# Performance work log

Hardware: AMD Instinct MI355X
Metric: run time of the kernel (lower is better)

## Reference

```python
import jax, jax.numpy as jnp
import numpy as np

N, D, E, L = 50000, 128, 800000, 3
BN_EPS = 1e-5


def _bn(h, mean, var, gamma, beta):
    # eval-mode BatchNorm1d with running statistics
    return (h - mean) * jax.lax.rsqrt(var + BN_EPS) * gamma + beta


def setup_inputs() -> dict:
    key = jax.random.key(0)
    ks = jax.random.split(key, 16)
    x = jax.random.normal(ks[0], (N, D), dtype=jnp.float32)
    edge_index = jax.random.randint(ks[1], (2, E), 0, N, dtype=jnp.int32)
    s = 1.0 / np.sqrt(D)
    W1 = jax.random.uniform(ks[2], (L, D, 2 * D), jnp.float32, -s, s)
    b1 = jax.random.uniform(ks[3], (L, 2 * D), jnp.float32, -s, s)
    g1 = jnp.ones((L, 2 * D), jnp.float32)
    be1 = jnp.zeros((L, 2 * D), jnp.float32)
    m1 = jax.random.normal(ks[4], (L, 2 * D), jnp.float32) * 0.1
    v1 = jax.random.uniform(ks[5], (L, 2 * D), jnp.float32, 0.5, 1.5)
    s2 = 1.0 / np.sqrt(2 * D)
    W2 = jax.random.uniform(ks[6], (L, 2 * D, D), jnp.float32, -s2, s2)
    b2 = jax.random.uniform(ks[7], (L, D), jnp.float32, -s2, s2)
    eps = jnp.zeros((L,), jnp.float32)  # train_eps=True, init 0
    go = jnp.ones((L - 1, D), jnp.float32)
    bo = jnp.zeros((L - 1, D), jnp.float32)
    mo = jax.random.normal(ks[8], (L - 1, D), jnp.float32) * 0.1
    vo = jax.random.uniform(ks[9], (L - 1, D), jnp.float32, 0.5, 1.5)
    return {"x": x, "edge_index": edge_index, "W1": W1, "b1": b1, "g1": g1,
            "be1": be1, "m1": m1, "v1": v1, "W2": W2, "b2": b2, "eps": eps,
            "go": go, "bo": bo, "mo": mo, "vo": vo}


def reference(x, edge_index, W1, b1, g1, be1, m1, v1, W2, b2, eps, go, bo, mo, vo):
    src, dst = edge_index[0], edge_index[1]
    n = x.shape[0]
    h = x
    for i in range(L):
        # GINConv: (1+eps)*x_i + sum_{j in N(i)} x_j, then MLP
        agg = jax.ops.segment_sum(h[src], dst, num_segments=n)  # [N, D]
        z = (1.0 + eps[i]) * h + agg
        z = jax.nn.relu(_bn(z @ W1[i] + b1[i], m1[i], v1[i], g1[i], be1[i]))
        z = z @ W2[i] + b2[i]
        if i < L - 1:
            z = jax.nn.relu(_bn(z, mo[i], vo[i], go[i], bo[i]))
            # dropout: identity in eval mode
        h = z
    return jax.nn.log_softmax(h, axis=-1)
```

## Files before the change

### kernel.cpp

```cpp
#include <hip/hip_runtime.h>

#define N_NODES 50000
#define DIM 128
#define E_EDGES 800000
#define L_LAYERS 3
#define MTPAD 3128
#define NBUCK 98
#define BCAP 9216
#define BSHIFT 9

#define CVT_BLOCKS 6250
#define TRANS_BLOCKS 768
#define PREP_BLOCKS 5

typedef __attribute__((ext_vector_type(4))) float f32x4;
typedef __attribute__((ext_vector_type(2))) _Float16 f16x2;
typedef __attribute__((ext_vector_type(4))) _Float16 f16x4;
typedef __attribute__((ext_vector_type(8))) _Float16 f16x8;

__device__ inline unsigned int pack4_fp8(float a, float b, float c, float d) {
    int pk = __builtin_amdgcn_cvt_pk_fp8_f32(a, b, 0, false);
    pk = __builtin_amdgcn_cvt_pk_fp8_f32(c, d, pk, true);
    return (unsigned int)pk;
}

__global__ __launch_bounds__(256) void setup_kernel(
        const float4* __restrict__ x4, f16x4* __restrict__ h16o,
        unsigned int* __restrict__ h8o,
        const float* __restrict__ w1, const float* __restrict__ w2,
        _Float16* __restrict__ f1, _Float16* __restrict__ f2,
        const float* __restrict__ b1, const float* __restrict__ g1,
        const float* __restrict__ be1, const float* __restrict__ m1,
        const float* __restrict__ v1, const float* __restrict__ b2,
        const float* __restrict__ go, const float* __restrict__ bo,
        const float* __restrict__ mo, const float* __restrict__ vo,
        float* __restrict__ scale1, float* __restrict__ shift1,
        float* __restrict__ scale2, float* __restrict__ shift2,
        int* __restrict__ gcur) {
    const int b = blockIdx.x;
    const int t = threadIdx.x;
    if (b < CVT_BLOCKS) {
        int i = b * 256 + t;
        float4 v = x4[i];
        f16x4 o;
        o[0] = (_Float16)v.x; o[1] = (_Float16)v.y;
        o[2] = (_Float16)v.z; o[3] = (_Float16)v.w;
        h16o[i] = o;
        h8o[i] = pack4_fp8(v.x, v.y, v.z, v.w);
    } else if (b < CVT_BLOCKS + TRANS_BLOCKS) {
        int idx = (b - CVT_BLOCKS) * 256 + t;
        const int per = DIM * 2 * DIM;
        const int tot = L_LAYERS * per;
        const float* w;
        _Float16* f;
        int K, Nn, id;
        if (idx < tot) { w = w1; f = f1; K = DIM; Nn = 2 * DIM; id = idx; }
        else           { w = w2; f = f2; K = 2 * DIM; Nn = DIM; id = idx - tot; }
        int l = id / per;
        int r = id - l * per;
        int k = r / Nn;
        int n = r - k * Nn;
        int KS = K >> 5;
        int off = ((((n >> 4) * KS + (k >> 5)) * 4 + ((k >> 3) & 3)) * 16 + (n & 15)) * 8 + (k & 7);
        f[(size_t)l * per + off] = (_Float16)w[id];
    } else if (b < CVT_BLOCKS + TRANS_BLOCKS + PREP_BLOCKS) {
        int idx = (b - (CVT_BLOCKS + TRANS_BLOCKS)) * 256 + t;
        if (idx < L_LAYERS * 256) {
            float sv = g1[idx] * rsqrtf(v1[idx] + 1e-5f);
            scale1[idx] = sv;
            shift1[idx] = (b1[idx] - m1[idx]) * sv + be1[idx];
        }
        int idx2 = idx - L_LAYERS * 256;
        if (idx2 >= 0 && idx2 < L_LAYERS * 128) {
            int l = idx2 >> 7;
            if (l < L_LAYERS - 1) {
                float sv = go[idx2] * rsqrtf(vo[idx2] + 1e-5f);
                scale2[idx2] = sv;
                shift2[idx2] = (b2[idx2] - mo[idx2]) * sv + bo[idx2];
            } else {
                scale2[idx2] = 1.0f;
                shift2[idx2] = b2[idx2];
            }
        }
    } else {
        if (t < NBUCK) gcur[t] = t * BCAP;
    }
}


__global__ __launch_bounds__(256) void bin_kernel(const int* __restrict__ ei,
                                                  int* __restrict__ gcur,
                                                  unsigned int* __restrict__ brec) {
    __shared__ int cnt[NBUCK];
    __shared__ int off[NBUCK];
    __shared__ int gbase[NBUCK];
    __shared__ unsigned int rec[4096];
    const int t = threadIdx.x;
    const int start = blockIdx.x * 4096;
    for (int i = t; i < NBUCK; i += 256) cnt[i] = 0;
    __syncthreads();
    unsigned int myrec[16];
    unsigned int mypos[16];
    int nmine = 0;
    #pragma unroll
    for (int i = 0; i < 16; ++i) {
        int e = start + i * 256 + t;
        if (e < E_EDGES) {
            int src = ei[e];
            int dst = ei[E_EDGES + e];
            int b = dst >> BSHIFT;
            int idx = atomicAdd(&cnt[b], 1);
            myrec[i] = ((unsigned int)(dst & 511) << 16) | (unsigned int)src;
            mypos[i] = ((unsigned int)b << 16) | (unsigned int)idx;
            nmine = i + 1;
        }
    }
    __syncthreads();
    if (t == 0) {
        int s = 0;
        for (int b = 0; b < NBUCK; ++b) { off[b] = s; s += cnt[b]; }
    }
    __syncthreads();
    #pragma unroll
    for (int i = 0; i < 16; ++i) {
        if (i < nmine) {
            int b = mypos[i] >> 16;
            int idx = mypos[i] & 0xFFFF;
            rec[off[b] + idx] = myrec[i];
        }
    }
    __syncthreads();
    if (t < NBUCK && cnt[t] > 0) gbase[t] = atomicAdd(&gcur[t], cnt[t]);
    __syncthreads();
    const int wv = t >> 6, lane = t & 63;
    for (int b = wv; b < NBUCK; b += 4) {
        int c = cnt[b], o = off[b], g = gbase[b];
        for (int j = lane; j < c; j += 64)
            brec[g + j] = rec[o + j];
    }
}

__global__ __launch_bounds__(256) void bsort_kernel(const unsigned int* __restrict__ brec,
                                                    const int* __restrict__ gcur,
                                                    int* __restrict__ rowp,
                                                    unsigned short* __restrict__ col) {
    __shared__ int ncnt[512];
    __shared__ int noff[512];
    __shared__ int wsum[4];
    __shared__ unsigned short srcbuf[BCAP];
    const int b = blockIdx.x;
    const int t = threadIdx.x;
    const int lane = t & 63;
    const int wv = t >> 6;
    int pv = (t < b) ? (gcur[t] - t * BCAP) : 0;
    #pragma unroll
    for (int d = 1; d < 64; d <<= 1) pv += __shfl_xor(pv, d, 64);
    if (lane == 0) wsum[wv] = pv;
    if (b == 0 && t == 0) rowp[N_NODES] = E_EDGES;
    const int cnt = gcur[b] - b * BCAP;
    const unsigned int* r = brec + (size_t)b * BCAP;
    for (int i = t; i < 512; i += 256) ncnt[i] = 0;
    __syncthreads();
    const int cb = wsum[0] + wsum[1] + wsum[2] + wsum[3];
    for (int j = t; j < cnt; j += 256)
        atomicAdd(&ncnt[r[j] >> 16], 1);
    __syncthreads();
    int a0 = ncnt[2 * t], a1 = ncnt[2 * t + 1];
    int pair = a0 + a1;
    int inc = pair;
    #pragma unroll
    for (int d = 1; d < 64; d <<= 1) {
        int u = __shfl_up(inc, d, 64);
        if (lane >= d) inc += u;
    }
    if (lane == 63) wsum[wv] = inc;
    __syncthreads();
    int wo = 0;
    if (wv > 0) wo = wsum[0];
    if (wv > 1) wo += wsum[1];
    if (wv > 2) wo += wsum[2];
    int excl = wo + inc - pair;
    noff[2 * t] = excl;
    noff[2 * t + 1] = excl + a0;
    __syncthreads();
    const int n0 = b << BSHIFT;
    for (int i = t; i < 512; i += 256) {
        int node = n0 + i;
        if (node < N_NODES) rowp[node] = cb + noff[i];
    }
    for (int i = t; i < 512; i += 256) ncnt[i] = noff[i];
    __syncthreads();
    for (int j = t; j < cnt; j += 256) {
        unsigned int v = r[j];
        int pos = atomicAdd(&ncnt[v >> 16], 1);
        srcbuf[pos] = (unsigned short)(v & 0xFFFFu);
    }
    __syncthreads();
    unsigned short* cp = col + cb;
    for (int j = t; j < cnt; j += 256) cp[j] = srcbuf[j];
}

__global__ __launch_bounds__(256) void aggregate_kernel(
        const unsigned int* __restrict__ h16,
        const unsigned int* __restrict__ h8,
        const int* __restrict__ row, const unsigned short* __restrict__ col,
        const float* __restrict__ epsp,
        unsigned short* __restrict__ zf) {
    const int wv = threadIdx.x >> 6;
    const int lane = threadIdx.x & 63;
    const int half = lane >> 5;
    const int m = lane & 31;
    const int node = blockIdx.x * 4 + wv;
    const f16x4* __restrict__ h4 = (const f16x4*)h16;
    const float s = 1.0f + epsp[0];
    f16x4 hv = h4[(size_t)node * 32 + m];
    float h0 = (float)hv[0], h1 = (float)hv[1], h2 = (float)hv[2], h3 = (float)hv[3];
    const int self8 = (int)h8[(size_t)node * 32 + m];
    float n0 = __builtin_amdgcn_cvt_f32_fp8(self8, 0);
    float n1 = __builtin_amdgcn_cvt_f32_fp8(self8, 1);
    float n2 = __builtin_amdgcn_cvt_f32_fp8(self8, 2);
    float n3 = __builtin_amdgcn_cvt_f32_fp8(self8, 3);
    float a0 = 0.f, a1 = 0.f, a2 = 0.f, a3 = 0.f;
    const int e0 = row[node], e1 = row[node + 1];
    int pad = 0;
    for (int e = e0; e < e1; e += 16) {
        int idx[8];
        #pragma unroll
        for (int p = 0; p < 8; ++p) {
            int ee = e + 2 * p + half;
            int cl = ee < E_EDGES - 1 ? ee : E_EDGES - 1;
            int cc = col[cl];
            idx[p] = (ee < e1) ? cc : node;
        }
        pad += (e + 16 > e1) ? (e + 16 - e1) : 0;
        int w0 = (int)h8[(size_t)idx[0] * 32 + m];
        int w1 = (int)h8[(size_t)idx[1] * 32 + m];
        int w2 = (int)h8[(size_t)idx[2] * 32 + m];
        int w3 = (int)h8[(size_t)idx[3] * 32 + m];
        int w4 = (int)h8[(size_t)idx[4] * 32 + m];
        int w5 = (int)h8[(size_t)idx[5] * 32 + m];
        int w6 = (int)h8[(size_t)idx[6] * 32 + m];
        int w7 = (int)h8[(size_t)idx[7] * 32 + m];
        a0 += ((__builtin_amdgcn_cvt_f32_fp8(w0, 0) + __builtin_amdgcn_cvt_f32_fp8(w1, 0))
             + (__builtin_amdgcn_cvt_f32_fp8(w2, 0) + __builtin_amdgcn_cvt_f32_fp8(w3, 0)))
            + ((__builtin_amdgcn_cvt_f32_fp8(w4, 0) + __builtin_amdgcn_cvt_f32_fp8(w5, 0))
             + (__builtin_amdgcn_cvt_f32_fp8(w6, 0) + __builtin_amdgcn_cvt_f32_fp8(w7, 0)));
        a1 += ((__builtin_amdgcn_cvt_f32_fp8(w0, 1) + __builtin_amdgcn_cvt_f32_fp8(w1, 1))
             + (__builtin_amdgcn_cvt_f32_fp8(w2, 1) + __builtin_amdgcn_cvt_f32_fp8(w3, 1)))
            + ((__builtin_amdgcn_cvt_f32_fp8(w4, 1) + __builtin_amdgcn_cvt_f32_fp8(w5, 1))
             + (__builtin_amdgcn_cvt_f32_fp8(w6, 1) + __builtin_amdgcn_cvt_f32_fp8(w7, 1)));
        a2 += ((__builtin_amdgcn_cvt_f32_fp8(w0, 2) + __builtin_amdgcn_cvt_f32_fp8(w1, 2))
             + (__builtin_amdgcn_cvt_f32_fp8(w2, 2) + __builtin_amdgcn_cvt_f32_fp8(w3, 2)))
            + ((__builtin_amdgcn_cvt_f32_fp8(w4, 2) + __builtin_amdgcn_cvt_f32_fp8(w5, 2))
             + (__builtin_amdgcn_cvt_f32_fp8(w6, 2) + __builtin_amdgcn_cvt_f32_fp8(w7, 2)));
        a3 += ((__builtin_amdgcn_cvt_f32_fp8(w0, 3) + __builtin_amdgcn_cvt_f32_fp8(w1, 3))
             + (__builtin_amdgcn_cvt_f32_fp8(w2, 3) + __builtin_amdgcn_cvt_f32_fp8(w3, 3)))
            + ((__builtin_amdgcn_cvt_f32_fp8(w4, 3) + __builtin_amdgcn_cvt_f32_fp8(w5, 3))
             + (__builtin_amdgcn_cvt_f32_fp8(w6, 3) + __builtin_amdgcn_cvt_f32_fp8(w7, 3)));
    }
    a0 += __shfl_xor(a0, 32, 64);
    a1 += __shfl_xor(a1, 32, 64);
    a2 += __shfl_xor(a2, 32, 64);
    a3 += __shfl_xor(a3, 32, 64);
    const float fpad = (float)pad;
    float t0 = s * h0 + a0 - fpad * n0;
    float t1 = s * h1 + a1 - fpad * n1;
    float t2 = s * h2 + a2 - fpad * n2;
    float t3 = s * h3 + a3 - fpad * n3;
    if (half == 0) {
        unsigned int lo = (unsigned int)__builtin_bit_cast(unsigned short, (_Float16)t0)
                        | ((unsigned int)__builtin_bit_cast(unsigned short, (_Float16)t1) << 16);
        unsigned int hi = (unsigned int)__builtin_bit_cast(unsigned short, (_Float16)t2)
                        | ((unsigned int)__builtin_bit_cast(unsigned short, (_Float16)t3) << 16);
        int mt = node >> 4, r16 = node & 15;
        int ks = m >> 3, quad = (m >> 1) & 3, j0 = (m & 1) * 4;
        size_t zo = (((size_t)(mt * 4 + ks)) * 4 + quad) * 128 + r16 * 8 + j0;
        uint2 pk; pk.x = lo; pk.y = hi;
        *(uint2*)(zf + zo) = pk;
    }
}

__global__ __launch_bounds__(256) void mlp_kernel(
        const _Float16* __restrict__ zf,
        const _Float16* __restrict__ w1f, const _Float16* __restrict__ w2f,
        const float* __restrict__ scale1, const float* __restrict__ shift1,
        const float* __restrict__ scale2, const float* __restrict__ shift2,
        int last,
        unsigned short* __restrict__ h16out, unsigned char* __restrict__ h8out,
        float* __restrict__ lsout) {
    __shared__ _Float16 wbuf[16384];
    __shared__ _Float16 tbuf[4][2][2048];
    const int tid = threadIdx.x;
    const int wave = tid >> 6;
    const int lane = tid & 63;
    const int quad = lane >> 4;
    const int l16 = lane & 15;
    const int mt0 = blockIdx.x * 8 + wave * 2;

    f16x8 ah[2][4];
    #pragma unroll
    for (int tt = 0; tt < 2; ++tt)
        #pragma unroll
        for (int ks = 0; ks < 4; ++ks)
            ah[tt][ks] = *(const f16x8*)(zf + (((size_t)((mt0 + tt) * 4 + ks)) << 9) + lane * 8);

    f32x4 acc2[2][8] = {};
    #pragma unroll
    for (int c = 0; c < 2; ++c) {
        {
            const _Float16* g = w1f + c * 16384 + tid * 8;
            _Float16* l = wbuf + tid * 8;
            #pragma unroll
            for (int j = 0; j < 8; ++j)
                *(f16x8*)(l + j * 2048) = *(const f16x8*)(g + j * 2048);
        }
        __syncthreads();
        #pragma unroll
        for (int ntl = 0; ntl < 8; ++ntl) {
            f32x4 acc[2] = {};
            #pragma unroll
            for (int ks = 0; ks < 4; ++ks) {
                f16x8 bfr = *(const f16x8*)&wbuf[(ntl * 4 + ks) * 512 + lane * 8];
                acc[0] = __builtin_amdgcn_mfma_f32_16x16x32_f16(ah[0][ks], bfr, acc[0], 0, 0, 0);
                acc[1] = __builtin_amdgcn_mfma_f32_16x16x32_f16(ah[1][ks], bfr, acc[1], 0, 0, 0);
            }
            int cg = (c * 8 + ntl) * 16 + l16;
            float sc = scale1[cg];
            float sh = shift1[cg];
            int plane = (cg >> 3) & 15;
            int basei = plane * 128 + (cg & 7);
            #pragma unroll
            for (int tt = 0; tt < 2; ++tt)
                #pragma unroll
                for (int r = 0; r < 4; ++r) {
                    float val = fmaxf(acc[tt][r] * sc + sh, 0.0f);
                    tbuf[wave][tt][basei + (quad * 4 + r) * 8] = (_Float16)val;
                }
        }
        __syncthreads();
        {
            #pragma unroll
            for (int nt = 0; nt < 8; ++nt) {
                *(f16x8*)&wbuf[nt * 2048 + tid * 8] =
                    *(const f16x8*)(w2f + (((size_t)(nt * 8 + c * 4)) << 9) + tid * 8);
            }
        }
        __syncthreads();
        #pragma unroll
        for (int ks4 = 0; ks4 < 4; ++ks4) {
            int po = (ks4 * 4 + quad) * 128 + l16 * 8;
            f16x8 a2_0 = *(const f16x8*)&tbuf[wave][0][po];
            f16x8 a2_1 = *(const f16x8*)&tbuf[wave][1][po];
            #pragma unroll
            for (int nt = 0; nt < 8; ++nt) {
                f16x8 bfr = *(const f16x8*)&wbuf[(nt * 4 + ks4) * 512 + lane * 8];
                acc2[0][nt] = __builtin_amdgcn_mfma_f32_16x16x32_f16(a2_0, bfr, acc2[0][nt], 0, 0, 0);
                acc2[1][nt] = __builtin_amdgcn_mfma_f32_16x16x32_f16(a2_1, bfr, acc2[1][nt], 0, 0, 0);
            }
        }
        __syncthreads();
    }

    #pragma unroll
    for (int nt = 0; nt < 8; ++nt) {
        int cg = nt * 16 + l16;
        float sc = scale2[cg];
        float sh = shift2[cg];
        #pragma unroll
        for (int tt = 0; tt < 2; ++tt)
            #pragma unroll
            for (int r = 0; r < 4; ++r)
                acc2[tt][nt][r] = acc2[tt][nt][r] * sc + sh;
    }
    if (!last) {
        #pragma unroll
        for (int tt = 0; tt < 2; ++tt) {
            const int R0 = (mt0 + tt) * 16;
            #pragma unroll
            for (int nt = 0; nt < 8; ++nt) {
                int cg = nt * 16 + l16;
                #pragma unroll
                for (int r = 0; r < 4; ++r) {
                    int rg = R0 + quad * 4 + r;
                    if (rg < N_NODES) {
                        float val = fmaxf(acc2[tt][nt][r], 0.0f);
                        h16out[(size_t)rg * DIM + cg] =
                            __builtin_bit_cast(unsigned short, (_Float16)val);
                        unsigned int pk = (unsigned int)
                            __builtin_amdgcn_cvt_pk_fp8_f32(val, 0.0f, 0, false);
                        h8out[(size_t)rg * DIM + cg] = (unsigned char)(pk & 0xFF);
                    }
                }
            }
        }
    } else {
        #pragma unroll
        for (int tt = 0; tt < 2; ++tt) {
            const int R0 = (mt0 + tt) * 16;
            #pragma unroll
            for (int r = 0; r < 4; ++r) {
                float mx = acc2[tt][0][r];
                #pragma unroll
                for (int nt = 1; nt < 8; ++nt) mx = fmaxf(mx, acc2[tt][nt][r]);
                #pragma unroll
                for (int off = 1; off < 16; off <<= 1) mx = fmaxf(mx, __shfl_xor(mx, off, 64));
                float sum = 0.0f;
                #pragma unroll
                for (int nt = 0; nt < 8; ++nt) sum += expf(acc2[tt][nt][r] - mx);
                #pragma unroll
                for (int off = 1; off < 16; off <<= 1) sum += __shfl_xor(sum, off, 64);
                float ls = mx + logf(sum);
                int rg = R0 + quad * 4 + r;
                if (rg < N_NODES) {
                    #pragma unroll
                    for (int nt = 0; nt < 8; ++nt)
                        lsout[(size_t)rg * DIM + nt * 16 + l16] = acc2[tt][nt][r] - ls;
                }
            }
        }
    }
}

extern "C" void kernel_launch(void* const* d_in, const int* in_sizes, int n_in,
                              void* d_out, int out_size, void* d_ws, size_t ws_size,
                              hipStream_t stream) {
    const float* x   = (const float*)d_in[0];
    const int*   ei  = (const int*)d_in[1];
    const float* W1  = (const float*)d_in[2];
    const float* b1  = (const float*)d_in[3];
    const float* g1  = (const float*)d_in[4];
    const float* be1 = (const float*)d_in[5];
    const float* m1  = (const float*)d_in[6];
    const float* v1  = (const float*)d_in[7];
    const float* W2  = (const float*)d_in[8];
    const float* b2  = (const float*)d_in[9];
    const float* eps = (const float*)d_in[10];
    const float* go  = (const float*)d_in[11];
    const float* bo  = (const float*)d_in[12];
    const float* mo  = (const float*)d_in[13];
    const float* vo  = (const float*)d_in[14];

    char* ws = (char*)d_ws;
    unsigned short* h16 = (unsigned short*)ws;  ws += (size_t)N_NODES * DIM * 2;
    unsigned char* h8 = (unsigned char*)ws;     ws += (size_t)N_NODES * DIM;
    unsigned short* zf = (unsigned short*)ws;   ws += (size_t)MTPAD * 2048 * 2;
    _Float16* w1f = (_Float16*)ws;              ws += (size_t)L_LAYERS * 32768 * 2;
    _Float16* w2f = (_Float16*)ws;              ws += (size_t)L_LAYERS * 32768 * 2;
    float* scale1 = (float*)ws; ws += (size_t)L_LAYERS * 256 * 4;
    float* shift1 = (float*)ws; ws += (size_t)L_LAYERS * 256 * 4;
    float* scale2 = (float*)ws; ws += (size_t)L_LAYERS * 128 * 4;
    float* shift2 = (float*)ws; ws += (size_t)L_LAYERS * 128 * 4;
    unsigned int* brec = (unsigned int*)ws; ws += (size_t)NBUCK * BCAP * 4;
    int* gcur = (int*)ws; ws += 128 * 4;
    int* rowp = (int*)ws; ws += (size_t)(N_NODES + 1) * 4;
    unsigned short* col = (unsigned short*)ws; ws += (size_t)E_EDGES * 2;

    setup_kernel<<<CVT_BLOCKS + TRANS_BLOCKS + PREP_BLOCKS + 1, 256, 0, stream>>>(
        (const float4*)x, (f16x4*)h16, (unsigned int*)h8, W1, W2, w1f, w2f,
        b1, g1, be1, m1, v1, b2, go, bo, mo, vo,
        scale1, shift1, scale2, shift2, gcur);
    bin_kernel<<<(E_EDGES + 4095) / 4096, 256, 0, stream>>>(ei, gcur, brec);
    bsort_kernel<<<NBUCK, 256, 0, stream>>>(brec, gcur, rowp, col);

    for (int i = 0; i < L_LAYERS; ++i) {
        aggregate_kernel<<<N_NODES / 4, 256, 0, stream>>>((const unsigned int*)h16,
                                                          (const unsigned int*)h8,
                                                          rowp, col, eps + i, zf);
        int last = (i == L_LAYERS - 1) ? 1 : 0;
        mlp_kernel<<<MTPAD / 8, 256, 0, stream>>>((const _Float16*)zf,
            w1f + (size_t)i * 32768, w2f + (size_t)i * 32768,
            scale1 + i * 256, shift1 + i * 256,
            scale2 + i * 128, shift2 + i * 128,
            last, h16, h8, (float*)d_out);
    }
}
```

Before: 271.0 us.

## Split fp8 feature table into column halves to shrink aggregation gather footprint

The fp8 neighbor-feature table is stored as two separate 64-column halves, written that way by setup and by the MLP epilogue. The aggregation launches twice as many blocks, each gathering from only one half with 16 lanes per row and 4 neighbors per wave step. The aim is to shrink the working set of the random gather so it stays in cache, at the cost of reading the CSR indices and row pointers twice. The bucket sort kernel also moves to 512 threads per block, and the padding count is now derived from the node degree.

```diff
diff --git a/kernel.cpp b/kernel.cpp
--- a/kernel.cpp
+++ b/kernel.cpp
@@ -26,7 +26,7 @@
 
 __global__ __launch_bounds__(256) void setup_kernel(
         const float4* __restrict__ x4, f16x4* __restrict__ h16o,
-        unsigned int* __restrict__ h8o,
+        unsigned int* __restrict__ h8a, unsigned int* __restrict__ h8b,
         const float* __restrict__ w1, const float* __restrict__ w2,
         _Float16* __restrict__ f1, _Float16* __restrict__ f2,
         const float* __restrict__ b1, const float* __restrict__ g1,
@@ -46,7 +46,10 @@
         o[0] = (_Float16)v.x; o[1] = (_Float16)v.y;
         o[2] = (_Float16)v.z; o[3] = (_Float16)v.w;
         h16o[i] = o;
-        h8o[i] = pack4_fp8(v.x, v.y, v.z, v.w);
+        unsigned int pk = pack4_fp8(v.x, v.y, v.z, v.w);
+        int node = i >> 5, d4 = i & 31;
+        if (d4 < 16) h8a[node * 16 + d4] = pk;
+        else         h8b[node * 16 + d4 - 16] = pk;
     } else if (b < CVT_BLOCKS + TRANS_BLOCKS) {
         int idx = (b - CVT_BLOCKS) * 256 + t;
         const int per = DIM * 2 * DIM;
@@ -140,13 +143,13 @@
     }
 }
 
-__global__ __launch_bounds__(256) void bsort_kernel(const unsigned int* __restrict__ brec,
+__global__ __launch_bounds__(512) void bsort_kernel(const unsigned int* __restrict__ brec,
                                                     const int* __restrict__ gcur,
                                                     int* __restrict__ rowp,
                                                     unsigned short* __restrict__ col) {
     __shared__ int ncnt[512];
     __shared__ int noff[512];
-    __shared__ int wsum[4];
+    __shared__ int wsum[8];
     __shared__ unsigned short srcbuf[BCAP];
     const int b = blockIdx.x;
     const int t = threadIdx.x;
@@ -159,121 +162,120 @@
     if (b == 0 && t == 0) rowp[N_NODES] = E_EDGES;
     const int cnt = gcur[b] - b * BCAP;
     const unsigned int* r = brec + (size_t)b * BCAP;
-    for (int i = t; i < 512; i += 256) ncnt[i] = 0;
-    __syncthreads();
-    const int cb = wsum[0] + wsum[1] + wsum[2] + wsum[3];
-    for (int j = t; j < cnt; j += 256)
+    for (int i = t; i < 512; i += 512) ncnt[i] = 0;
+    __syncthreads();
+    int cb = 0;
+    #pragma unroll
+    for (int k = 0; k < 8; ++k) cb += wsum[k];
+    for (int j = t; j < cnt; j += 512)
         atomicAdd(&ncnt[r[j] >> 16], 1);
     __syncthreads();
-    int a0 = ncnt[2 * t], a1 = ncnt[2 * t + 1];
-    int pair = a0 + a1;
-    int inc = pair;
-    #pragma unroll
-    for (int d = 1; d < 64; d <<= 1) {
-        int u = __shfl_up(inc, d, 64);
-        if (lane >= d) inc += u;
-    }
-    if (lane == 63) wsum[wv] = inc;
-    __syncthreads();
-    int wo = 0;
-    if (wv > 0) wo = wsum[0];
-    if (wv > 1) wo += wsum[1];
-    if (wv > 2) wo += wsum[2];
-    int excl = wo + inc - pair;
-    noff[2 * t] = excl;
-    noff[2 * t + 1] = excl + a0;
+    if (t < 256) {
+        int a0 = ncnt[2 * t], a1 = ncnt[2 * t + 1];
+        int pair = a0 + a1;
+        int inc = pair;
+        #pragma unroll
+        for (int d = 1; d < 64; d <<= 1) {
+            int u = __shfl_up(inc, d, 64);
+            if (lane >= d) inc += u;
+        }
+        if (lane == 63) wsum[wv] = inc;
+        __syncthreads();
+        int wo = 0;
+        if (wv > 0) wo = wsum[0];
+        if (wv > 1) wo += wsum[1];
+        if (wv > 2) wo += wsum[2];
+        int excl = wo + inc - pair;
+        noff[2 * t] = excl;
+        noff[2 * t + 1] = excl + a0;
+    } else {
+        __syncthreads();
+    }
     __syncthreads();
     const int n0 = b << BSHIFT;
-    for (int i = t; i < 512; i += 256) {
+    {
+        int i = t;
         int node = n0 + i;
         if (node < N_NODES) rowp[node] = cb + noff[i];
-    }
-    for (int i = t; i < 512; i += 256) ncnt[i] = noff[i];
-    __syncthreads();
-    for (int j = t; j < cnt; j += 256) {
+        ncnt[i] = noff[i];
+    }
+    __syncthreads();
+    for (int j = t; j < cnt; j += 512) {
         unsigned int v = r[j];
         int pos = atomicAdd(&ncnt[v >> 16], 1);
         srcbuf[pos] = (unsigned short)(v & 0xFFFFu);
     }
     __syncthreads();
     unsigned short* cp = col + cb;
-    for (int j = t; j < cnt; j += 256) cp[j] = srcbuf[j];
+    for (int j = t; j < cnt; j += 512) cp[j] = srcbuf[j];
 }
 
 __global__ __launch_bounds__(256) void aggregate_kernel(
         const unsigned int* __restrict__ h16,
-        const unsigned int* __restrict__ h8,
+        const unsigned int* __restrict__ h8a,
+        const unsigned int* __restrict__ h8b,
         const int* __restrict__ row, const unsigned short* __restrict__ col,
         const float* __restrict__ epsp,
         unsigned short* __restrict__ zf) {
     const int wv = threadIdx.x >> 6;
     const int lane = threadIdx.x & 63;
-    const int half = lane >> 5;
-    const int m = lane & 31;
-    const int node = blockIdx.x * 4 + wv;
+    const int q = lane >> 4;
+    const int m16 = lane & 15;
+    const int bid = blockIdx.x;
+    const int g = (bid >= 12500) ? 1 : 0;
+    const int node = (g ? (bid - 12500) : bid) * 4 + wv;
+    const unsigned int* __restrict__ h8x = g ? h8b : h8a;
+    const int cgd = g * 16 + m16;
     const f16x4* __restrict__ h4 = (const f16x4*)h16;
     const float s = 1.0f + epsp[0];
-    f16x4 hv = h4[(size_t)node * 32 + m];
+    f16x4 hv = h4[(size_t)node * 32 + cgd];
     float h0 = (float)hv[0], h1 = (float)hv[1], h2 = (float)hv[2], h3 = (float)hv[3];
-    const int self8 = (int)h8[(size_t)node * 32 + m];
+    const int self8 = (int)h8x[(size_t)node * 16 + m16];
     float n0 = __builtin_amdgcn_cvt_f32_fp8(self8, 0);
     float n1 = __builtin_amdgcn_cvt_f32_fp8(self8, 1);
     float n2 = __builtin_amdgcn_cvt_f32_fp8(self8, 2);
     float n3 = __builtin_amdgcn_cvt_f32_fp8(self8, 3);
     float a0 = 0.f, a1 = 0.f, a2 = 0.f, a3 = 0.f;
     const int e0 = row[node], e1 = row[node + 1];
-    int pad = 0;
     for (int e = e0; e < e1; e += 16) {
-        int idx[8];
-        #pragma unroll
-        for (int p = 0; p < 8; ++p) {
-            int ee = e + 2 * p + half;
+        int idx[4];
+        #pragma unroll
+        for (int p = 0; p < 4; ++p) {
+            int ee = e + 4 * p + q;
             int cl = ee < E_EDGES - 1 ? ee : E_EDGES - 1;
             int cc = col[cl];
             idx[p] = (ee < e1) ? cc : node;
         }
-        pad += (e + 16 > e1) ? (e + 16 - e1) : 0;
-        int w0 = (int)h8[(size_t)idx[0] * 32 + m];
-        int w1 = (int)h8[(size_t)idx[1] * 32 + m];
-        int w2 = (int)h8[(size_t)idx[2] * 32 + m];
-        int w3 = (int)h8[(size_t)idx[3] * 32 + m];
-        int w4 = (int)h8[(size_t)idx[4] * 32 + m];
-        int w5 = (int)h8[(size_t)idx[5] * 32 + m];
-        int w6 = (int)h8[(size_t)idx[6] * 32 + m];
-        int w7 = (int)h8[(size_t)idx[7] * 32 + m];
-        a0 += ((__builtin_amdgcn_cvt_f32_fp8(w0, 0) + __builtin_amdgcn_cvt_f32_fp8(w1, 0))
-             + (__builtin_amdgcn_cvt_f32_fp8(w2, 0) + __builtin_amdgcn_cvt_f32_fp8(w3, 0)))
-            + ((__builtin_amdgcn_cvt_f32_fp8(w4, 0) + __builtin_amdgcn_cvt_f32_fp8(w5, 0))
-             + (__builtin_amdgcn_cvt_f32_fp8(w6, 0) + __builtin_amdgcn_cvt_f32_fp8(w7, 0)));
-        a1 += ((__builtin_amdgcn_cvt_f32_fp8(w0, 1) + __builtin_amdgcn_cvt_f32_fp8(w1, 1))
-             + (__builtin_amdgcn_cvt_f32_fp8(w2, 1) + __builtin_amdgcn_cvt_f32_fp8(w3, 1)))
-            + ((__builtin_amdgcn_cvt_f32_fp8(w4, 1) + __builtin_amdgcn_cvt_f32_fp8(w5, 1))
-             + (__builtin_amdgcn_cvt_f32_fp8(w6, 1) + __builtin_amdgcn_cvt_f32_fp8(w7, 1)));
-        a2 += ((__builtin_amdgcn_cvt_f32_fp8(w0, 2) + __builtin_amdgcn_cvt_f32_fp8(w1, 2))
-             + (__builtin_amdgcn_cvt_f32_fp8(w2, 2) + __builtin_amdgcn_cvt_f32_fp8(w3, 2)))
-            + ((__builtin_amdgcn_cvt_f32_fp8(w4, 2) + __builtin_amdgcn_cvt_f32_fp8(w5, 2))
-             + (__builtin_amdgcn_cvt_f32_fp8(w6, 2) + __builtin_amdgcn_cvt_f32_fp8(w7, 2)));
-        a3 += ((__builtin_amdgcn_cvt_f32_fp8(w0, 3) + __builtin_amdgcn_cvt_f32_fp8(w1, 3))
-             + (__builtin_amdgcn_cvt_f32_fp8(w2, 3) + __builtin_amdgcn_cvt_f32_fp8(w3, 3)))
-            + ((__builtin_amdgcn_cvt_f32_fp8(w4, 3) + __builtin_amdgcn_cvt_f32_fp8(w5, 3))
-             + (__builtin_amdgcn_cvt_f32_fp8(w6, 3) + __builtin_amdgcn_cvt_f32_fp8(w7, 3)));
-    }
-    a0 += __shfl_xor(a0, 32, 64);
-    a1 += __shfl_xor(a1, 32, 64);
-    a2 += __shfl_xor(a2, 32, 64);
-    a3 += __shfl_xor(a3, 32, 64);
-    const float fpad = (float)pad;
+        int w0 = (int)h8x[(size_t)idx[0] * 16 + m16];
+        int w1 = (int)h8x[(size_t)idx[1] * 16 + m16];
+        int w2 = (int)h8x[(size_t)idx[2] * 16 + m16];
+        int w3 = (int)h8x[(size_t)idx[3] * 16 + m16];
+        a0 += (__builtin_amdgcn_cvt_f32_fp8(w0, 0) + __builtin_amdgcn_cvt_f32_fp8(w1, 0))
+            + (__builtin_amdgcn_cvt_f32_fp8(w2, 0) + __builtin_amdgcn_cvt_f32_fp8(w3, 0));
+        a1 += (__builtin_amdgcn_cvt_f32_fp8(w0, 1) + __builtin_amdgcn_cvt_f32_fp8(w1, 1))
+            + (__builtin_amdgcn_cvt_f32_fp8(w2, 1) + __builtin_amdgcn_cvt_f32_fp8(w3, 1));
+        a2 += (__builtin_amdgcn_cvt_f32_fp8(w0, 2) + __builtin_amdgcn_cvt_f32_fp8(w1, 2))
+            + (__builtin_amdgcn_cvt_f32_fp8(w2, 2) + __builtin_amdgcn_cvt_f32_fp8(w3, 2));
+        a3 += (__builtin_amdgcn_cvt_f32_fp8(w0, 3) + __builtin_amdgcn_cvt_f32_fp8(w1, 3))
+            + (__builtin_amdgcn_cvt_f32_fp8(w2, 3) + __builtin_amdgcn_cvt_f32_fp8(w3, 3));
+    }
+    a0 += __shfl_xor(a0, 16, 64); a0 += __shfl_xor(a0, 32, 64);
+    a1 += __shfl_xor(a1, 16, 64); a1 += __shfl_xor(a1, 32, 64);
+    a2 += __shfl_xor(a2, 16, 64); a2 += __shfl_xor(a2, 32, 64);
+    a3 += __shfl_xor(a3, 16, 64); a3 += __shfl_xor(a3, 32, 64);
+    const int deg = e1 - e0;
+    const float fpad = (float)(((deg + 15) & ~15) - deg);
     float t0 = s * h0 + a0 - fpad * n0;
     float t1 = s * h1 + a1 - fpad * n1;
     float t2 = s * h2 + a2 - fpad * n2;
     float t3 = s * h3 + a3 - fpad * n3;
-    if (half == 0) {
+    if (q == 0) {
         unsigned int lo = (unsigned int)__builtin_bit_cast(unsigned short, (_Float16)t0)
                         | ((unsigned int)__builtin_bit_cast(unsigned short, (_Float16)t1) << 16);
         unsigned int hi = (unsigned int)__builtin_bit_cast(unsigned short, (_Float16)t2)
                         | ((unsigned int)__builtin_bit_cast(unsigned short, (_Float16)t3) << 16);
         int mt = node >> 4, r16 = node & 15;
-        int ks = m >> 3, quad = (m >> 1) & 3, j0 = (m & 1) * 4;
+        int ks = cgd >> 3, quad = (cgd >> 1) & 3, j0 = (cgd & 1) * 4;
         size_t zo = (((size_t)(mt * 4 + ks)) * 4 + quad) * 128 + r16 * 8 + j0;
         uint2 pk; pk.x = lo; pk.y = hi;
         *(uint2*)(zf + zo) = pk;
@@ -286,7 +288,8 @@
         const float* __restrict__ scale1, const float* __restrict__ shift1,
         const float* __restrict__ scale2, const float* __restrict__ shift2,
         int last,
-        unsigned short* __restrict__ h16out, unsigned char* __restrict__ h8out,
+        unsigned short* __restrict__ h16out,
+        unsigned char* __restrict__ h8aout, unsigned char* __restrict__ h8bout,
         float* __restrict__ lsout) {
     __shared__ _Float16 wbuf[16384];
     __shared__ _Float16 tbuf[4][2][2048];
@@ -388,7 +391,9 @@
                             __builtin_bit_cast(unsigned short, (_Float16)val);
                         unsigned int pk = (unsigned int)
                             __builtin_amdgcn_cvt_pk_fp8_f32(val, 0.0f, 0, false);
-                        h8out[(size_t)rg * DIM + cg] = (unsigned char)(pk & 0xFF);
+                        unsigned char byv = (unsigned char)(pk & 0xFF);
+                        if (nt < 4) h8aout[(size_t)rg * 64 + cg] = byv;
+                        else        h8bout[(size_t)rg * 64 + cg - 64] = byv;
                     }
                 }
             }
@@ -442,7 +447,8 @@
 
     char* ws = (char*)d_ws;
     unsigned short* h16 = (unsigned short*)ws;  ws += (size_t)N_NODES * DIM * 2;
-    unsigned char* h8 = (unsigned char*)ws;     ws += (size_t)N_NODES * DIM;
+    unsigned char* h8a = (unsigned char*)ws;    ws += (size_t)N_NODES * 64;
+    unsigned char* h8b = (unsigned char*)ws;    ws += (size_t)N_NODES * 64;
     unsigned short* zf = (unsigned short*)ws;   ws += (size_t)MTPAD * 2048 * 2;
     _Float16* w1f = (_Float16*)ws;              ws += (size_t)L_LAYERS * 32768 * 2;
     _Float16* w2f = (_Float16*)ws;              ws += (size_t)L_LAYERS * 32768 * 2;
@@ -456,21 +462,23 @@
     unsigned short* col = (unsigned short*)ws; ws += (size_t)E_EDGES * 2;
 
     setup_kernel<<<CVT_BLOCKS + TRANS_BLOCKS + PREP_BLOCKS + 1, 256, 0, stream>>>(
-        (const float4*)x, (f16x4*)h16, (unsigned int*)h8, W1, W2, w1f, w2f,
+        (const float4*)x, (f16x4*)h16, (unsigned int*)h8a, (unsigned int*)h8b,
+        W1, W2, w1f, w2f,
         b1, g1, be1, m1, v1, b2, go, bo, mo, vo,
         scale1, shift1, scale2, shift2, gcur);
     bin_kernel<<<(E_EDGES + 4095) / 4096, 256, 0, stream>>>(ei, gcur, brec);
-    bsort_kernel<<<NBUCK, 256, 0, stream>>>(brec, gcur, rowp, col);
+    bsort_kernel<<<NBUCK, 512, 0, stream>>>(brec, gcur, rowp, col);
 
     for (int i = 0; i < L_LAYERS; ++i) {
-        aggregate_kernel<<<N_NODES / 4, 256, 0, stream>>>((const unsigned int*)h16,
-                                                          (const unsigned int*)h8,
-                                                          rowp, col, eps + i, zf);
+        aggregate_kernel<<<25000, 256, 0, stream>>>((const unsigned int*)h16,
+                                                    (const unsigned int*)h8a,
+                                                    (const unsigned int*)h8b,
+                                                    rowp, col, eps + i, zf);
         int last = (i == L_LAYERS - 1) ? 1 : 0;
         mlp_kernel<<<MTPAD / 8, 256, 0, stream>>>((const _Float16*)zf,
             w1f + (size_t)i * 32768, w2f + (size_t)i * 32768,
             scale1 + i * 256, shift1 + i * 256,
             scale2 + i * 128, shift2 + i * 128,
-            last, h16, h8, (float*)d_out);
-    }
-}
+            last, h16, h8a, h8b, (float*)d_out);
+    }
+}
```

Result: slower. 295.4 us (+9.0%).
